# Performance work log

Measured on AMD Instinct MI355X. Metric: run time of the kernel, lower is better.

## Reference

```python
import jax, jax.numpy as jnp
import numpy as np

B, C, N = 8, 256, 2048

def setup_inputs() -> dict:
    key = jax.random.key(0)
    ks = jax.random.split(key, 7)
    s = 1.0 / np.sqrt(C)
    return {
        "x": jax.random.normal(ks[0], (B, C, N), dtype=jnp.float32),
        "Wq": jax.random.normal(ks[1], (C, C), dtype=jnp.float32) * s,
        "bq": jax.random.normal(ks[2], (C,), dtype=jnp.float32) * s,
        "Wk": jax.random.normal(ks[3], (C, C), dtype=jnp.float32) * s,
        "bk": jax.random.normal(ks[4], (C,), dtype=jnp.float32) * s,
        "Wv": jax.random.normal(ks[5], (C, C), dtype=jnp.float32) * s,
        "bv": jax.random.normal(ks[6], (C,), dtype=jnp.float32) * s,
    }

def reference(x, Wq, bq, Wk, bk, Wv, bv):
    # x: [B, C, N]; Conv1d(k=1) == channel-mixing matmul + bias
    q = jnp.einsum('oc,bcn->bon', Wq, x) + bq[None, :, None]  # [B,C,N]
    k = jnp.einsum('oc,bcn->bon', Wk, x) + bk[None, :, None]  # [B,C,N]
    v = jnp.einsum('oc,bcn->bon', Wv, x) + bv[None, :, None]  # [B,C,N]
    # qk = bmm(q^T, k): [B, N, N]
    qk = jnp.einsum('bcn,bcm->bnm', q, k)
    # global-sum normalization over the ENTIRE qk tensor (not row-wise softmax)
    attn_w = qk / jnp.sum(qk)
    # attn = bmm(v, attn_w): [B, C, N]
    attn = jnp.einsum('bcn,bnm->bcm', v, attn_w)
    return attn
```

## Files before the change

### kernel.cpp

```cpp
#include <hip/hip_runtime.h>


typedef _Float16 half8 __attribute__((ext_vector_type(8)));
typedef _Float16 half4 __attribute__((ext_vector_type(4)));
typedef _Float16 half2v __attribute__((ext_vector_type(2)));
typedef float f4v __attribute__((ext_vector_type(4)));

#define GP  40
#define GPB 36

__launch_bounds__(256)
__global__ void k1_kernel(const float* __restrict__ x, const float* __restrict__ Wq,
                          const float* __restrict__ Wk, const float* __restrict__ bq,
                          const float* __restrict__ bk, float* __restrict__ sxpart,
                          float* __restrict__ W3, float* __restrict__ u2,
                          float* __restrict__ w1, float* __restrict__ s1,
                          float* __restrict__ S, float* __restrict__ Gpart) {
    __shared__ __align__(16) char smem[40960];
    const int blk = blockIdx.x, t = threadIdx.x;
    if (blk < 192) {
        _Float16* Ah = (_Float16*)smem;
        _Float16* Al = Ah + 128 * GP;
        _Float16* Bh = Al + 128 * GP;
        _Float16* Bl = Bh + 128 * GP;
        const int tileId = blk >> 6;
        const int y = blk & 63;
        const int b = y >> 3, ks = y & 7;
        const int r0 = (tileId == 2) ? 128 : 0;
        const int c0 = (tileId == 0) ? 0 : 128;
        const bool diag = (tileId != 1);
        const float* xb = x + (long)b * 524288;

        const int lane = t & 63, wave = t >> 6;
        const int wy = wave >> 1, wx = wave & 1;
        const int mIn = lane & 15, quad = lane >> 4;

        f4v acc[4][4] = {};
        const int aBase = (wy * 64 + mIn) * GP + quad * 8;
        const int bBase = (wx * 64 + mIn) * GP + quad * 8;
        const int srow = t >> 3;
        const int skq  = (t & 7) * 4;
        float rs[4] = {};

        float4 pa[4], pb[4];
        int kk = ks * 256;
        #pragma unroll
        for (int i = 0; i < 4; ++i) {
            pa[i] = *(const float4*)&xb[(long)(r0 + srow + i * 32) * 2048 + kk + skq];
            if (!diag) pb[i] = *(const float4*)&xb[(long)(c0 + srow + i * 32) * 2048 + kk + skq];
        }

        for (int kb = 0; kb < 8; ++kb) {
            if (kb) __syncthreads();
            #pragma unroll
            for (int i = 0; i < 4; ++i) {
                const int row = srow + i * 32;
                half4 hv, lv;
                hv[0] = (_Float16)pa[i].x; lv[0] = (_Float16)(pa[i].x - (float)hv[0]);
                hv[1] = (_Float16)pa[i].y; lv[1] = (_Float16)(pa[i].y - (float)hv[1]);
                hv[2] = (_Float16)pa[i].z; lv[2] = (_Float16)(pa[i].z - (float)hv[2]);
                hv[3] = (_Float16)pa[i].w; lv[3] = (_Float16)(pa[i].w - (float)hv[3]);
                *(half4*)&Ah[row * GP + skq] = hv;
                *(half4*)&Al[row * GP + skq] = lv;
                if (diag) {
                    rs[i] += pa[i].x + pa[i].y + pa[i].z + pa[i].w;
                } else {
                    half4 hb, lb;
                    hb[0] = (_Float16)pb[i].x; lb[0] = (_Float16)(pb[i].x - (float)hb[0]);
                    hb[1] = (_Float16)pb[i].y; lb[1] = (_Float16)(pb[i].y - (float)hb[1]);
                    hb[2] = (_Float16)pb[i].z; lb[2] = (_Float16)(pb[i].z - (float)hb[2]);
                    hb[3] = (_Float16)pb[i].w; lb[3] = (_Float16)(pb[i].w - (float)hb[3]);
                    *(half4*)&Bh[row * GP + skq] = hb;
                    *(half4*)&Bl[row * GP + skq] = lb;
                }
            }
            __syncthreads();
            kk += 32;
            if (kb < 7) {
                #pragma unroll
                for (int i = 0; i < 4; ++i) {
                    pa[i] = *(const float4*)&xb[(long)(r0 + srow + i * 32) * 2048 + kk + skq];
                    if (!diag) pb[i] = *(const float4*)&xb[(long)(c0 + srow + i * 32) * 2048 + kk + skq];
                }
            }
            const _Float16* BhP = diag ? Ah : Bh;
            const _Float16* BlP = diag ? Al : Bl;
            #pragma unroll
            for (int ph = 0; ph < 3; ++ph) {
                const _Float16* As = (ph == 2) ? Al : Ah;
                const _Float16* Bs = (ph == 1) ? BlP : BhP;
                half8 af[4], bf[4];
                #pragma unroll
                for (int i = 0; i < 4; ++i) {
                    af[i] = *(const half8*)&As[aBase + i * 16 * GP];
                    bf[i] = *(const half8*)&Bs[bBase + i * 16 * GP];
                }
                #pragma unroll
                for (int i = 0; i < 4; ++i)
                    #pragma unroll
                    for (int j = 0; j < 4; ++j)
                        acc[i][j] = __builtin_amdgcn_mfma_f32_16x16x32_f16(af[i], bf[j], acc[i][j], 0, 0, 0);
            }
        }

        if (diag) {
            #pragma unroll
            for (int i = 0; i < 4; ++i) {
                rs[i] += __shfl_xor(rs[i], 1);
                rs[i] += __shfl_xor(rs[i], 2);
                rs[i] += __shfl_xor(rs[i], 4);
            }
            if ((t & 7) == 0) {
                #pragma unroll
                for (int i = 0; i < 4; ++i)
                    sxpart[ks * 2048 + b * 256 + r0 + srow + i * 32] = rs[i];
            }
        }

        float* D = Gpart + ((long)(ks * 8 + b) << 16);
        #pragma unroll
        for (int i = 0; i < 4; ++i)
            #pragma unroll
            for (int j = 0; j < 4; ++j) {
                const int row = r0 + wy * 64 + i * 16 + quad * 4;
                const int col = c0 + wx * 64 + j * 16 + mIn;
                #pragma unroll
                for (int r = 0; r < 4; ++r)
                    D[(row + r) * 256 + col] = acc[i][j][r];
                if (tileId == 1)
                    *(float4*)&D[(long)col * 256 + row] =
                        make_float4(acc[i][j][0], acc[i][j][1], acc[i][j][2], acc[i][j][3]);
            }
    } else if (blk < 208) {
        float* ldsA = (float*)smem;
        float* ldsB = ldsA + 16 * 68;
        const int tile = blk - 192;
        const int r0 = (tile >> 2) * 64, j0 = (tile & 3) * 64;
        const int tx = t & 15, ty = t >> 4;
        float acc[4][4] = {};
        for (int kk = 0; kk < 256; kk += 16) {
            *(float4*)&ldsA[ty * 68 + tx * 4] = *(const float4*)&Wq[(long)(kk + ty) * 256 + r0 + tx * 4];
            *(float4*)&ldsB[ty * 68 + tx * 4] = *(const float4*)&Wk[(long)(kk + ty) * 256 + j0 + tx * 4];
            __syncthreads();
            #pragma unroll
            for (int k = 0; k < 16; ++k) {
                const float4 av4 = *(const float4*)&ldsA[k * 68 + ty * 4];
                const float4 bv4 = *(const float4*)&ldsB[k * 68 + tx * 4];
                const float ar[4] = {av4.x, av4.y, av4.z, av4.w};
                const float br[4] = {bv4.x, bv4.y, bv4.z, bv4.w};
                #pragma unroll
                for (int i = 0; i < 4; ++i)
                    #pragma unroll
                    for (int j = 0; j < 4; ++j)
                        acc[i][j] = fmaf(ar[i], br[j], acc[i][j]);
            }
            __syncthreads();
        }
        #pragma unroll
        for (int i = 0; i < 4; ++i)
            *(float4*)&W3[(long)(r0 + ty * 4 + i) * 256 + j0 + tx * 4] =
                make_float4(acc[i][0], acc[i][1], acc[i][2], acc[i][3]);
    } else {
        float* sbq = (float*)smem;
        float* sbk = sbq + 256;
        float* red = sbk + 256;
        if (t == 0) S[0] = 0.0f;
        sbq[t] = bq[t]; sbk[t] = bk[t];
        __syncthreads();
        float u = 0.0f, w = 0.0f;
        #pragma unroll 8
        for (int c = 0; c < 256; ++c) {
            u = fmaf(Wk[(long)c * 256 + t], sbq[c], u);
            w = fmaf(Wq[(long)c * 256 + t], sbk[c], w);
        }
        u2[t] = u; w1[t] = w;
        red[t] = sbq[t] * sbk[t]; __syncthreads();
        for (int h = 128; h > 0; h >>= 1) { if (t < h) red[t] += red[t + h]; __syncthreads(); }
        if (t == 0) s1[0] = red[0];
    }
}

__launch_bounds__(256)
__global__ void k2_kernel(const float* __restrict__ Wv, const float* __restrict__ Gpart,
                          const float* __restrict__ W3, const float* __restrict__ u2,
                          const float* __restrict__ w1, const float* __restrict__ s1p,
                          const float* __restrict__ sxpart, float* __restrict__ T1,
                          float* __restrict__ v2, float* __restrict__ s2,
                          float* __restrict__ wvsx, float* __restrict__ S) {
    __shared__ __align__(16) char smem[40960];
    const int blk = blockIdx.x, t = threadIdx.x;
    if (blk < 256) {
        float* ldsA = (float*)smem;
        float* ldsB = ldsA + 32 * 34;
        const int r0 = (blk >> 5) * 32;
        const int g  = blk & 31;
        const int b  = g >> 2;
        const int j0 = (g & 3) * 64;
        const int tx = t & 15, ty = t >> 4;
        const int ar = t >> 3, ak4 = (t & 7) * 4;
        const float* Gb = Gpart + (long)b * 65536 + j0;
        float acc[2][4] = {};

        f4v pa, pg[2][8];
        pa = *(const f4v*)&Wv[(long)(r0 + ar) * 256 + ak4];
        #pragma unroll
        for (int s = 0; s < 2; ++s)
            #pragma unroll
            for (int ksl = 0; ksl < 8; ++ksl)
                pg[s][ksl] = *(const f4v*)&Gb[(long)ksl * 524288 + (long)(s * 16 + ty) * 256 + tx * 4];

        for (int c = 0; c < 8; ++c) {
            const int kk = c * 32;
            ldsA[(ak4 + 0) * 34 + ar] = pa[0];
            ldsA[(ak4 + 1) * 34 + ar] = pa[1];
            ldsA[(ak4 + 2) * 34 + ar] = pa[2];
            ldsA[(ak4 + 3) * 34 + ar] = pa[3];
            #pragma unroll
            for (int s = 0; s < 2; ++s) {
                f4v bs = pg[s][0];
                #pragma unroll
                for (int ksl = 1; ksl < 8; ++ksl) bs += pg[s][ksl];
                *(f4v*)&ldsB[(s * 16 + ty) * 68 + tx * 4] = bs;
            }
            __syncthreads();
            if (c < 7) {
                const int kn = kk + 32;
                pa = *(const f4v*)&Wv[(long)(r0 + ar) * 256 + kn + ak4];
                #pragma unroll
                for (int s = 0; s < 2; ++s)
                    #pragma unroll
                    for (int ksl = 0; ksl < 8; ++ksl)
                        pg[s][ksl] = *(const f4v*)&Gb[(long)ksl * 524288 + (long)(kn + s * 16 + ty) * 256 + tx * 4];
            }
            #pragma unroll
            for (int k = 0; k < 32; ++k) {
                const float2 av2 = *(const float2*)&ldsA[k * 34 + ty * 2];
                const float4 bv4 = *(const float4*)&ldsB[k * 68 + tx * 4];
                acc[0][0] = fmaf(av2.x, bv4.x, acc[0][0]);
                acc[0][1] = fmaf(av2.x, bv4.y, acc[0][1]);
                acc[0][2] = fmaf(av2.x, bv4.z, acc[0][2]);
                acc[0][3] = fmaf(av2.x, bv4.w, acc[0][3]);
                acc[1][0] = fmaf(av2.y, bv4.x, acc[1][0]);
                acc[1][1] = fmaf(av2.y, bv4.y, acc[1][1]);
                acc[1][2] = fmaf(av2.y, bv4.z, acc[1][2]);
                acc[1][3] = fmaf(av2.y, bv4.w, acc[1][3]);
            }
            __syncthreads();
        }
        float* D = T1 + (long)b * 65536;
        #pragma unroll
        for (int i = 0; i < 2; ++i)
            *(float4*)&D[(long)(r0 + ty * 2 + i) * 256 + j0 + tx * 4] =
                make_float4(acc[i][0], acc[i][1], acc[i][2], acc[i][3]);
    } else if (blk < 264) {
        float* ssx = (float*)smem;
        float* red = ssx + 256;
        const int b = blk - 256, j = t;
        float sxv = 0.0f;
        #pragma unroll
        for (int ks = 0; ks < 8; ++ks) sxv += sxpart[ks * 2048 + b * 256 + j];
        ssx[j] = sxv;
        __syncthreads();
        float vr = 0.0f;
        #pragma unroll 8
        for (int c = 0; c < 256; ++c) vr = fmaf(W3[(long)c * 256 + j], ssx[c], vr);
        const float v2j = vr + 2048.0f * u2[j];
        v2[b * 256 + j] = v2j;
        red[j] = v2j * sxv; __syncthreads();
        for (int h = 128; h > 0; h >>= 1) { if (j < h) red[j] += red[j + h]; __syncthreads(); }
        const float sd1 = red[0];
        __syncthreads();
        red[j] = sxv * w1[j]; __syncthreads();
        for (int h = 128; h > 0; h >>= 1) { if (j < h) red[j] += red[j + h]; __syncthreads(); }
        if (j == 0) {
            const float s2v = red[0] + 2048.0f * s1p[0];
            s2[b] = s2v;
            atomicAdd(S, sd1 + 2048.0f * s2v);
        }
    } else {
        float* wtile = (float*)smem;
        float* sxs = wtile + 8192;
        const int r0w = (blk - 264) * 32;
        #pragma unroll
        for (int p = 0; p < 8; ++p) {
            const int f = t + p * 256;
            const int row = f >> 6, c4 = f & 63;
            *(float4*)&wtile[row * 256 + c4 * 4] = *(const float4*)&Wv[(long)(r0w + row) * 256 + c4 * 4];
        }
        #pragma unroll
        for (int p = 0; p < 8; ++p) {
            const int f = t + p * 256;
            float s = 0.0f;
            #pragma unroll
            for (int ks = 0; ks < 8; ++ks) s += sxpart[ks * 2048 + f];
            sxs[f] = s;
        }
        __syncthreads();
        const int r = t >> 3, q = t & 7;
        float acc[8] = {};
        for (int ci = 0; ci < 32; ++ci) {
            const float wv = wtile[r * 256 + q * 32 + ci];
            #pragma unroll
            for (int b = 0; b < 8; ++b) acc[b] = fmaf(wv, sxs[b * 256 + q * 32 + ci], acc[b]);
        }
        #pragma unroll
        for (int b = 0; b < 8; ++b) {
            acc[b] += __shfl_xor(acc[b], 1);
            acc[b] += __shfl_xor(acc[b], 2);
            acc[b] += __shfl_xor(acc[b], 4);
        }
        if (q == 0) {
            #pragma unroll
            for (int b = 0; b < 8; ++b) wvsx[b * 256 + r0w + r] = acc[b];
        }
    }
}

__launch_bounds__(256)
__global__ void ap_kernel(const float* __restrict__ T1, const float* __restrict__ W3,
                          const float* __restrict__ wvsx, const float* __restrict__ u2,
                          const float* __restrict__ bv, const float* __restrict__ v2,
                          const float* __restrict__ w1, const float* __restrict__ s1p,
                          const float* __restrict__ s2, _Float16* __restrict__ Aph,
                          _Float16* __restrict__ Apl, float* __restrict__ cvec) {
    __shared__ __align__(16) float ldsA[32 * 34];
    __shared__ __align__(16) float ldsB[32 * 68];
    __shared__ float sw1[256];
    const int b = blockIdx.z;
    const int r0 = blockIdx.y * 32, j0 = blockIdx.x * 64;
    const float* A = T1 + (long)b * 65536;
    const int t = threadIdx.x, tx = t & 15, ty = t >> 4;
    const int ar = t >> 3, ak4 = (t & 7) * 4;
    sw1[t] = w1[t];
    float acc[2][4] = {};
    float dot[2] = {};

    f4v pa, pb[2];
    pa = *(const f4v*)&A[(long)(r0 + ar) * 256 + ak4];
    pb[0] = *(const f4v*)&W3[(long)(ty) * 256 + j0 + tx * 4];
    pb[1] = *(const f4v*)&W3[(long)(16 + ty) * 256 + j0 + tx * 4];

    for (int c = 0; c < 8; ++c) {
        const int kk = c * 32;
        ldsA[(ak4 + 0) * 34 + ar] = pa[0];
        ldsA[(ak4 + 1) * 34 + ar] = pa[1];
        ldsA[(ak4 + 2) * 34 + ar] = pa[2];
        ldsA[(ak4 + 3) * 34 + ar] = pa[3];
        *(f4v*)&ldsB[ty * 68 + tx * 4] = pb[0];
        *(f4v*)&ldsB[(16 + ty) * 68 + tx * 4] = pb[1];
        __syncthreads();
        if (c < 7) {
            const int kn = kk + 32;
            pa = *(const f4v*)&A[(long)(r0 + ar) * 256 + kn + ak4];
            pb[0] = *(const f4v*)&W3[(long)(kn + ty) * 256 + j0 + tx * 4];
            pb[1] = *(const f4v*)&W3[(long)(kn + 16 + ty) * 256 + j0 + tx * 4];
        }
        #pragma unroll
        for (int k = 0; k < 32; ++k) {
            const float2 av2 = *(const float2*)&ldsA[k * 34 + ty * 2];
            const float4 bv4 = *(const float4*)&ldsB[k * 68 + tx * 4];
            const float wk = sw1[kk + k];
            dot[0] = fmaf(av2.x, wk, dot[0]);
            dot[1] = fmaf(av2.y, wk, dot[1]);
            acc[0][0] = fmaf(av2.x, bv4.x, acc[0][0]);
            acc[0][1] = fmaf(av2.x, bv4.y, acc[0][1]);
            acc[0][2] = fmaf(av2.x, bv4.z, acc[0][2]);
            acc[0][3] = fmaf(av2.x, bv4.w, acc[0][3]);
            acc[1][0] = fmaf(av2.y, bv4.x, acc[1][0]);
            acc[1][1] = fmaf(av2.y, bv4.y, acc[1][1]);
            acc[1][2] = fmaf(av2.y, bv4.z, acc[1][2]);
            acc[1][3] = fmaf(av2.y, bv4.w, acc[1][3]);
        }
        __syncthreads();
    }
    #pragma unroll
    for (int i = 0; i < 2; ++i) {
        const int r = r0 + ty * 2 + i;
        const float e1 = wvsx[b * 256 + r], e3 = bv[r];
        half4 hv, lv;
        #pragma unroll
        for (int j = 0; j < 4; ++j) {
            const int col = j0 + tx * 4 + j;
            const float val = acc[i][j] + e1 * u2[col] + e3 * v2[b * 256 + col];
            hv[j] = (_Float16)val;
            lv[j] = (_Float16)(val - (float)hv[j]);
        }
        const long o = (long)b * 65536 + (long)r * 256 + j0 + tx * 4;
        *(half4*)&Aph[o] = hv;
        *(half4*)&Apl[o] = lv;
        if (j0 == 0 && tx == 0)
            cvec[b * 256 + r] = dot[i] + e1 * s1p[0] + e3 * s2[b];
    }
}

__launch_bounds__(256)
__global__ void gemmF_mfma(const _Float16* __restrict__ Aph, const _Float16* __restrict__ Apl,
                           const float* __restrict__ x, const float* __restrict__ Sptr,
                           const float* __restrict__ cvec, float* __restrict__ out) {
    __shared__ __align__(16) _Float16 Ah[128 * GP];
    __shared__ __align__(16) _Float16 Al[128 * GP];
    __shared__ __align__(16) _Float16 Bh[128 * GPB];
    __shared__ __align__(16) _Float16 Bl[128 * GPB];
    __shared__ __align__(16) float xt[32 * 132];

    const int n0 = blockIdx.x * 128;
    const int c0 = blockIdx.y * 128;
    const int b = blockIdx.z;
    const _Float16* Asrc_h = Aph + (long)b * 65536;
    const _Float16* Asrc_l = Apl + (long)b * 65536;
    const float* xb = x + (long)b * 524288;

    const int t = threadIdx.x;
    const int lane = t & 63, wave = t >> 6;
    const int wy = wave >> 1, wx = wave & 1;
    const int mIn = lane & 15, quad = lane >> 4;

    f4v acc[4][4] = {};
    const int aBase = (wy * 64 + mIn) * GP + quad * 8;
    const int bBase = (wx * 64 + mIn) * GPB + quad * 8;
    const int cn = t & 127;
    const int ckh = (t >> 7) * 16;

    int arow[2], ako[2], xk[4], xn[4];
    #pragma unroll
    for (int i = 0; i < 2; ++i) { const int idx = t + (i << 8); arow[i] = idx >> 2; ako[i] = (idx & 3) << 3; }
    #pragma unroll
    for (int p = 0; p < 4; ++p) { const int f = t + p * 256; xk[p] = f >> 5; xn[p] = f & 31; }

    uint4 pah[2], pal[2]; f4v px[4];
    #pragma unroll
    for (int i = 0; i < 2; ++i) {
        pah[i] = *(const uint4*)&Asrc_h[(long)(c0 + arow[i]) * 256 + ako[i]];
        pal[i] = *(const uint4*)&Asrc_l[(long)(c0 + arow[i]) * 256 + ako[i]];
    }
    #pragma unroll
    for (int p = 0; p < 4; ++p)
        px[p] = *(const f4v*)&xb[(long)xk[p] * 2048 + n0 + xn[p] * 4];

    for (int kk = 0; kk < 256; kk += 32) {
        #pragma unroll
        for (int i = 0; i < 2; ++i) {
            *(uint4*)&Ah[arow[i] * GP + ako[i]] = pah[i];
            *(uint4*)&Al[arow[i] * GP + ako[i]] = pal[i];
        }
        #pragma unroll
        for (int p = 0; p < 4; ++p)
            *(f4v*)&xt[xk[p] * 132 + xn[p] * 4] = px[p];
        __syncthreads();
        {
            _Float16 hs[16], ls[16];
            #pragma unroll
            for (int k = 0; k < 16; ++k) {
                const float v = xt[(ckh + k) * 132 + cn];
                hs[k] = (_Float16)v;
                ls[k] = (_Float16)(v - (float)hs[k]);
            }
            #pragma unroll
            for (int k2 = 0; k2 < 8; ++k2) {
                half2v h2; h2[0] = hs[2 * k2]; h2[1] = hs[2 * k2 + 1];
                half2v l2; l2[0] = ls[2 * k2]; l2[1] = ls[2 * k2 + 1];
                *(half2v*)&Bh[cn * GPB + ckh + 2 * k2] = h2;
                *(half2v*)&Bl[cn * GPB + ckh + 2 * k2] = l2;
            }
        }
        __syncthreads();
        if (kk < 224) {
            const int kn = kk + 32;
            #pragma unroll
            for (int i = 0; i < 2; ++i) {
                pah[i] = *(const uint4*)&Asrc_h[(long)(c0 + arow[i]) * 256 + kn + ako[i]];
                pal[i] = *(const uint4*)&Asrc_l[(long)(c0 + arow[i]) * 256 + kn + ako[i]];
            }
            #pragma unroll
            for (int p = 0; p < 4; ++p)
                px[p] = *(const f4v*)&xb[(long)(kn + xk[p]) * 2048 + n0 + xn[p] * 4];
        }
        #pragma unroll
        for (int ph = 0; ph < 3; ++ph) {
            const _Float16* As = (ph == 2) ? Al : Ah;
            const _Float16* Bs = (ph == 1) ? Bl : Bh;
            half8 af[4], bf[4];
            #pragma unroll
            for (int i = 0; i < 4; ++i) {
                af[i] = *(const half8*)&As[aBase + i * 16 * GP];
                const half4 b0 = *(const half4*)&Bs[bBase + i * 16 * GPB];
                const half4 b1 = *(const half4*)&Bs[bBase + i * 16 * GPB + 4];
                bf[i] = __builtin_shufflevector(b0, b1, 0, 1, 2, 3, 4, 5, 6, 7);
            }
            #pragma unroll
            for (int i = 0; i < 4; ++i)
                #pragma unroll
                for (int j = 0; j < 4; ++j)
                    acc[i][j] = __builtin_amdgcn_mfma_f32_16x16x32_f16(af[i], bf[j], acc[i][j], 0, 0, 0);
        }
        __syncthreads();
    }

    const float invS = 1.0f / Sptr[0];
    float* ob = out + (long)b * 524288;
    const float* cv = cvec + b * 256;
    #pragma unroll
    for (int i = 0; i < 4; ++i)
        #pragma unroll
        for (int r = 0; r < 4; ++r) {
            const int row = c0 + wy * 64 + i * 16 + quad * 4 + r;
            const float c = cv[row];
            #pragma unroll
            for (int j = 0; j < 4; ++j) {
                const int col = n0 + wx * 64 + j * 16 + mIn;
                ob[(long)row * 2048 + col] = (acc[i][j][r] + c) * invS;
            }
        }
}

extern "C" void kernel_launch(void* const* d_in, const int* in_sizes, int n_in,
                              void* d_out, int out_size, void* d_ws, size_t ws_size,
                              hipStream_t stream) {
    const float* x  = (const float*)d_in[0];
    const float* Wq = (const float*)d_in[1];
    const float* bq = (const float*)d_in[2];
    const float* Wk = (const float*)d_in[3];
    const float* bk = (const float*)d_in[4];
    const float* Wv = (const float*)d_in[5];
    const float* bv = (const float*)d_in[6];
    float* out = (float*)d_out;
    float* ws  = (float*)d_ws;

    float* T1     = ws;
    float* W3     = ws + 524288;
    float* sxpart = ws + 589824;
    float* wvsx   = ws + 606208;
    float* v2     = ws + 608256;
    float* cvec   = ws + 610304;
    float* s2     = ws + 612352;
    float* u2     = ws + 612360;
    float* w1     = ws + 612616;
    float* s1     = ws + 612872;
    float* S      = ws + 612873;
    float* Gpart  = ws + 612880;
    _Float16* Aph = (_Float16*)(ws + 4807184);
    _Float16* Apl = Aph + 524288;

    k1_kernel<<<dim3(209), 256, 0, stream>>>(x, Wq, Wk, bq, bk, sxpart, W3, u2, w1, s1, S, Gpart);
    k2_kernel<<<dim3(272), 256, 0, stream>>>(Wv, Gpart, W3, u2, w1, s1, sxpart, T1, v2, s2, wvsx, S);
    ap_kernel<<<dim3(4, 8, 8), 256, 0, stream>>>(T1, W3, wvsx, u2, bv, v2, w1, s1, s2, Aph, Apl, cvec);
    gemmF_mfma<<<dim3(16, 2, 8), 256, 0, stream>>>(Aph, Apl, x, S, cvec, out);
}
```

Baseline: 154.3 us.

## Fuse four kernels into one persistent kernel with software grid barriers

Merges the four stage kernels into a single 256-block kernel whose phases are separated by atomic-counter grid barriers, with a memset resetting the barrier flags each launch. The aim is to remove the launch gaps and tail drain between the short dependent stages. The cost is that every block must be co-resident (256 blocks on 256 CUs), blocks spin while waiting, and stages with fewer blocks, such as the reduction ones, leave most of the grid idle at each barrier.

```diff
diff --git a/kernel.cpp b/kernel.cpp
--- a/kernel.cpp
+++ b/kernel.cpp
@@ -9,15 +9,38 @@
 #define GP  40
 #define GPB 36
 
-__launch_bounds__(256)
-__global__ void k1_kernel(const float* __restrict__ x, const float* __restrict__ Wq,
-                          const float* __restrict__ Wk, const float* __restrict__ bq,
-                          const float* __restrict__ bk, float* __restrict__ sxpart,
-                          float* __restrict__ W3, float* __restrict__ u2,
-                          float* __restrict__ w1, float* __restrict__ s1,
-                          float* __restrict__ S, float* __restrict__ Gpart) {
-    __shared__ __align__(16) char smem[40960];
+__device__ __forceinline__ void gbar(unsigned* cnt, unsigned* flag, unsigned nblk) {
+    __syncthreads();
+    if (threadIdx.x == 0) {
+        __threadfence();
+        if (__hip_atomic_fetch_add(cnt, 1u, __ATOMIC_RELAXED, __HIP_MEMORY_SCOPE_AGENT) == nblk - 1u) {
+            __hip_atomic_store(flag, 1u, __ATOMIC_RELAXED, __HIP_MEMORY_SCOPE_AGENT);
+        } else {
+            while (__hip_atomic_load(flag, __ATOMIC_RELAXED, __HIP_MEMORY_SCOPE_AGENT) == 0u)
+                __builtin_amdgcn_s_sleep(2);
+        }
+        __threadfence();
+    }
+    __syncthreads();
+}
+
+__launch_bounds__(256, 1)
+__global__ void fused_kernel(const float* __restrict__ x, const float* __restrict__ Wq,
+                             const float* __restrict__ bq, const float* __restrict__ Wk,
+                             const float* __restrict__ bk, const float* __restrict__ Wv,
+                             const float* __restrict__ bv, float* __restrict__ out,
+                             float* __restrict__ T1, float* __restrict__ W3,
+                             float* __restrict__ sxpart, float* __restrict__ wvsx,
+                             float* __restrict__ v2, float* __restrict__ cvec,
+                             float* __restrict__ s2, float* __restrict__ u2,
+                             float* __restrict__ w1, float* __restrict__ s1,
+                             float* __restrict__ S, float* __restrict__ Gpart,
+                             _Float16* __restrict__ Aph, _Float16* __restrict__ Apl,
+                             unsigned* __restrict__ bar) {
+    __shared__ __align__(16) char smem[55808];
     const int blk = blockIdx.x, t = threadIdx.x;
+    const unsigned NBLK = 256;
+
     if (blk < 192) {
         _Float16* Ah = (_Float16*)smem;
         _Float16* Al = Ah + 128 * GP;
@@ -160,7 +183,7 @@
         for (int i = 0; i < 4; ++i)
             *(float4*)&W3[(long)(r0 + ty * 4 + i) * 256 + j0 + tx * 4] =
                 make_float4(acc[i][0], acc[i][1], acc[i][2], acc[i][3]);
-    } else {
+    } else if (blk == 208) {
         float* sbq = (float*)smem;
         float* sbk = sbq + 256;
         float* red = sbk + 256;
@@ -178,18 +201,10 @@
         for (int h = 128; h > 0; h >>= 1) { if (t < h) red[t] += red[t + h]; __syncthreads(); }
         if (t == 0) s1[0] = red[0];
     }
-}
-
-__launch_bounds__(256)
-__global__ void k2_kernel(const float* __restrict__ Wv, const float* __restrict__ Gpart,
-                          const float* __restrict__ W3, const float* __restrict__ u2,
-                          const float* __restrict__ w1, const float* __restrict__ s1p,
-                          const float* __restrict__ sxpart, float* __restrict__ T1,
-                          float* __restrict__ v2, float* __restrict__ s2,
-                          float* __restrict__ wvsx, float* __restrict__ S) {
-    __shared__ __align__(16) char smem[40960];
-    const int blk = blockIdx.x, t = threadIdx.x;
-    if (blk < 256) {
+
+    gbar(&bar[0], &bar[1], NBLK);
+
+    {
         float* ldsA = (float*)smem;
         float* ldsB = ldsA + 32 * 34;
         const int r0 = (blk >> 5) * 32;
@@ -252,10 +267,12 @@
         for (int i = 0; i < 2; ++i)
             *(float4*)&D[(long)(r0 + ty * 2 + i) * 256 + j0 + tx * 4] =
                 make_float4(acc[i][0], acc[i][1], acc[i][2], acc[i][3]);
-    } else if (blk < 264) {
+    }
+    if (blk < 8) {
+        __syncthreads();
         float* ssx = (float*)smem;
         float* red = ssx + 256;
-        const int b = blk - 256, j = t;
+        const int b = blk, j = t;
         float sxv = 0.0f;
         #pragma unroll
         for (int ks = 0; ks < 8; ++ks) sxv += sxpart[ks * 2048 + b * 256 + j];
@@ -273,14 +290,15 @@
         red[j] = sxv * w1[j]; __syncthreads();
         for (int h = 128; h > 0; h >>= 1) { if (j < h) red[j] += red[j + h]; __syncthreads(); }
         if (j == 0) {
-            const float s2v = red[0] + 2048.0f * s1p[0];
+            const float s2v = red[0] + 2048.0f * s1[0];
             s2[b] = s2v;
             atomicAdd(S, sd1 + 2048.0f * s2v);
         }
-    } else {
+    } else if (blk < 16) {
+        __syncthreads();
         float* wtile = (float*)smem;
         float* sxs = wtile + 8192;
-        const int r0w = (blk - 264) * 32;
+        const int r0w = (blk - 8) * 32;
         #pragma unroll
         for (int p = 0; p < 8; ++p) {
             const int f = t + p * 256;
@@ -314,203 +332,197 @@
             for (int b = 0; b < 8; ++b) wvsx[b * 256 + r0w + r] = acc[b];
         }
     }
-}
-
-__launch_bounds__(256)
-__global__ void ap_kernel(const float* __restrict__ T1, const float* __restrict__ W3,
-                          const float* __restrict__ wvsx, const float* __restrict__ u2,
-                          const float* __restrict__ bv, const float* __restrict__ v2,
-                          const float* __restrict__ w1, const float* __restrict__ s1p,
-                          const float* __restrict__ s2, _Float16* __restrict__ Aph,
-                          _Float16* __restrict__ Apl, float* __restrict__ cvec) {
-    __shared__ __align__(16) float ldsA[32 * 34];
-    __shared__ __align__(16) float ldsB[32 * 68];
-    __shared__ float sw1[256];
-    const int b = blockIdx.z;
-    const int r0 = blockIdx.y * 32, j0 = blockIdx.x * 64;
-    const float* A = T1 + (long)b * 65536;
-    const int t = threadIdx.x, tx = t & 15, ty = t >> 4;
-    const int ar = t >> 3, ak4 = (t & 7) * 4;
-    sw1[t] = w1[t];
-    float acc[2][4] = {};
-    float dot[2] = {};
-
-    f4v pa, pb[2];
-    pa = *(const f4v*)&A[(long)(r0 + ar) * 256 + ak4];
-    pb[0] = *(const f4v*)&W3[(long)(ty) * 256 + j0 + tx * 4];
-    pb[1] = *(const f4v*)&W3[(long)(16 + ty) * 256 + j0 + tx * 4];
-
-    for (int c = 0; c < 8; ++c) {
-        const int kk = c * 32;
-        ldsA[(ak4 + 0) * 34 + ar] = pa[0];
-        ldsA[(ak4 + 1) * 34 + ar] = pa[1];
-        ldsA[(ak4 + 2) * 34 + ar] = pa[2];
-        ldsA[(ak4 + 3) * 34 + ar] = pa[3];
-        *(f4v*)&ldsB[ty * 68 + tx * 4] = pb[0];
-        *(f4v*)&ldsB[(16 + ty) * 68 + tx * 4] = pb[1];
-        __syncthreads();
-        if (c < 7) {
-            const int kn = kk + 32;
-            pa = *(const f4v*)&A[(long)(r0 + ar) * 256 + kn + ak4];
-            pb[0] = *(const f4v*)&W3[(long)(kn + ty) * 256 + j0 + tx * 4];
-            pb[1] = *(const f4v*)&W3[(long)(kn + 16 + ty) * 256 + j0 + tx * 4];
-        }
-        #pragma unroll
-        for (int k = 0; k < 32; ++k) {
-            const float2 av2 = *(const float2*)&ldsA[k * 34 + ty * 2];
-            const float4 bv4 = *(const float4*)&ldsB[k * 68 + tx * 4];
-            const float wk = sw1[kk + k];
-            dot[0] = fmaf(av2.x, wk, dot[0]);
-            dot[1] = fmaf(av2.y, wk, dot[1]);
-            acc[0][0] = fmaf(av2.x, bv4.x, acc[0][0]);
-            acc[0][1] = fmaf(av2.x, bv4.y, acc[0][1]);
-            acc[0][2] = fmaf(av2.x, bv4.z, acc[0][2]);
-            acc[0][3] = fmaf(av2.x, bv4.w, acc[0][3]);
-            acc[1][0] = fmaf(av2.y, bv4.x, acc[1][0]);
-            acc[1][1] = fmaf(av2.y, bv4.y, acc[1][1]);
-            acc[1][2] = fmaf(av2.y, bv4.z, acc[1][2]);
-            acc[1][3] = fmaf(av2.y, bv4.w, acc[1][3]);
-        }
-        __syncthreads();
+
+    gbar(&bar[2], &bar[3], NBLK);
+
+    {
+        float* ldsA = (float*)smem;
+        float* ldsB = (float*)(smem + 4352);
+        float* sw1  = (float*)(smem + 13056);
+        const int b  = blk >> 5;
+        const int r0 = ((blk >> 2) & 7) * 32, j0 = (blk & 3) * 64;
+        const float* A = T1 + (long)b * 65536;
+        const int tx = t & 15, ty = t >> 4;
+        const int ar = t >> 3, ak4 = (t & 7) * 4;
+        sw1[t] = w1[t];
+        float acc[2][4] = {};
+        float dot[2] = {};
+
+        f4v pa, pb[2];
+        pa = *(const f4v*)&A[(long)(r0 + ar) * 256 + ak4];
+        pb[0] = *(const f4v*)&W3[(long)(ty) * 256 + j0 + tx * 4];
+        pb[1] = *(const f4v*)&W3[(long)(16 + ty) * 256 + j0 + tx * 4];
+
+        for (int c = 0; c < 8; ++c) {
+            const int kk = c * 32;
+            ldsA[(ak4 + 0) * 34 + ar] = pa[0];
+            ldsA[(ak4 + 1) * 34 + ar] = pa[1];
+            ldsA[(ak4 + 2) * 34 + ar] = pa[2];
+            ldsA[(ak4 + 3) * 34 + ar] = pa[3];
+            *(f4v*)&ldsB[ty * 68 + tx * 4] = pb[0];
+            *(f4v*)&ldsB[(16 + ty) * 68 + tx * 4] = pb[1];
+            __syncthreads();
+            if (c < 7) {
+                const int kn = kk + 32;
+                pa = *(const f4v*)&A[(long)(r0 + ar) * 256 + kn + ak4];
+                pb[0] = *(const f4v*)&W3[(long)(kn + ty) * 256 + j0 + tx * 4];
+                pb[1] = *(const f4v*)&W3[(long)(kn + 16 + ty) * 256 + j0 + tx * 4];
+            }
+            #pragma unroll
+            for (int k = 0; k < 32; ++k) {
+                const float2 av2 = *(const float2*)&ldsA[k * 34 + ty * 2];
+                const float4 bv4 = *(const float4*)&ldsB[k * 68 + tx * 4];
+                const float wk = sw1[kk + k];
+                dot[0] = fmaf(av2.x, wk, dot[0]);
+                dot[1] = fmaf(av2.y, wk, dot[1]);
+                acc[0][0] = fmaf(av2.x, bv4.x, acc[0][0]);
+                acc[0][1] = fmaf(av2.x, bv4.y, acc[0][1]);
+                acc[0][2] = fmaf(av2.x, bv4.z, acc[0][2]);
+                acc[0][3] = fmaf(av2.x, bv4.w, acc[0][3]);
+                acc[1][0] = fmaf(av2.y, bv4.x, acc[1][0]);
+                acc[1][1] = fmaf(av2.y, bv4.y, acc[1][1]);
+                acc[1][2] = fmaf(av2.y, bv4.z, acc[1][2]);
+                acc[1][3] = fmaf(av2.y, bv4.w, acc[1][3]);
+            }
+            __syncthreads();
+        }
+        #pragma unroll
+        for (int i = 0; i < 2; ++i) {
+            const int r = r0 + ty * 2 + i;
+            const float e1 = wvsx[b * 256 + r], e3 = bv[r];
+            half4 hv, lv;
+            #pragma unroll
+            for (int j = 0; j < 4; ++j) {
+                const int col = j0 + tx * 4 + j;
+                const float val = acc[i][j] + e1 * u2[col] + e3 * v2[b * 256 + col];
+                hv[j] = (_Float16)val;
+                lv[j] = (_Float16)(val - (float)hv[j]);
+            }
+            const long o = (long)b * 65536 + (long)r * 256 + j0 + tx * 4;
+            *(half4*)&Aph[o] = hv;
+            *(half4*)&Apl[o] = lv;
+            if (j0 == 0 && tx == 0)
+                cvec[b * 256 + r] = dot[i] + e1 * s1[0] + e3 * s2[b];
+        }
     }
-    #pragma unroll
-    for (int i = 0; i < 2; ++i) {
-        const int r = r0 + ty * 2 + i;
-        const float e1 = wvsx[b * 256 + r], e3 = bv[r];
-        half4 hv, lv;
-        #pragma unroll
-        for (int j = 0; j < 4; ++j) {
-            const int col = j0 + tx * 4 + j;
-            const float val = acc[i][j] + e1 * u2[col] + e3 * v2[b * 256 + col];
-            hv[j] = (_Float16)val;
-            lv[j] = (_Float16)(val - (float)hv[j]);
-        }
-        const long o = (long)b * 65536 + (long)r * 256 + j0 + tx * 4;
-        *(half4*)&Aph[o] = hv;
-        *(half4*)&Apl[o] = lv;
-        if (j0 == 0 && tx == 0)
-            cvec[b * 256 + r] = dot[i] + e1 * s1p[0] + e3 * s2[b];
+
+    gbar(&bar[4], &bar[5], NBLK);
+
+    {
+        _Float16* Ah = (_Float16*)smem;
+        _Float16* Al = (_Float16*)(smem + 10240);
+        _Float16* Bh = (_Float16*)(smem + 20480);
+        _Float16* Bl = (_Float16*)(smem + 29696);
+        float*    xt = (float*)(smem + 38912);
+
+        const int n0 = (blk & 15) * 128;
+        const int c0 = ((blk >> 4) & 1) * 128;
+        const int b  = blk >> 5;
+        const _Float16* Asrc_h = Aph + (long)b * 65536;
+        const _Float16* Asrc_l = Apl + (long)b * 65536;
+        const float* xb = x + (long)b * 524288;
+
+        const int lane = t & 63, wave = t >> 6;
+        const int wy = wave >> 1, wx = wave & 1;
+        const int mIn = lane & 15, quad = lane >> 4;
+
+        f4v acc[4][4] = {};
+        const int aBase = (wy * 64 + mIn) * GP + quad * 8;
+        const int bBase = (wx * 64 + mIn) * GPB + quad * 8;
+        const int cn = t & 127;
+        const int ckh = (t >> 7) * 16;
+
+        int arow[2], ako[2], xk[4], xn[4];
+        #pragma unroll
+        for (int i = 0; i < 2; ++i) { const int idx = t + (i << 8); arow[i] = idx >> 2; ako[i] = (idx & 3) << 3; }
+        #pragma unroll
+        for (int p = 0; p < 4; ++p) { const int f = t + p * 256; xk[p] = f >> 5; xn[p] = f & 31; }
+
+        uint4 pah[2], pal[2]; f4v px[4];
+        #pragma unroll
+        for (int i = 0; i < 2; ++i) {
+            pah[i] = *(const uint4*)&Asrc_h[(long)(c0 + arow[i]) * 256 + ako[i]];
+            pal[i] = *(const uint4*)&Asrc_l[(long)(c0 + arow[i]) * 256 + ako[i]];
+        }
+        #pragma unroll
+        for (int p = 0; p < 4; ++p)
+            px[p] = *(const f4v*)&xb[(long)xk[p] * 2048 + n0 + xn[p] * 4];
+
+        for (int kk = 0; kk < 256; kk += 32) {
+            #pragma unroll
+            for (int i = 0; i < 2; ++i) {
+                *(uint4*)&Ah[arow[i] * GP + ako[i]] = pah[i];
+                *(uint4*)&Al[arow[i] * GP + ako[i]] = pal[i];
+            }
+            #pragma unroll
+            for (int p = 0; p < 4; ++p)
+                *(f4v*)&xt[xk[p] * 132 + xn[p] * 4] = px[p];
+            __syncthreads();
+            {
+                _Float16 hs[16], ls[16];
+                #pragma unroll
+                for (int k = 0; k < 16; ++k) {
+                    const float v = xt[(ckh + k) * 132 + cn];
+                    hs[k] = (_Float16)v;
+                    ls[k] = (_Float16)(v - (float)hs[k]);
+                }
+                #pragma unroll
+                for (int k2 = 0; k2 < 8; ++k2) {
+                    half2v h2; h2[0] = hs[2 * k2]; h2[1] = hs[2 * k2 + 1];
+                    half2v l2; l2[0] = ls[2 * k2]; l2[1] = ls[2 * k2 + 1];
+                    *(half2v*)&Bh[cn * GPB + ckh + 2 * k2] = h2;
+                    *(half2v*)&Bl[cn * GPB + ckh + 2 * k2] = l2;
+                }
+            }
+            __syncthreads();
+            if (kk < 224) {
+                const int kn = kk + 32;
+                #pragma unroll
+                for (int i = 0; i < 2; ++i) {
+                    pah[i] = *(const uint4*)&Asrc_h[(long)(c0 + arow[i]) * 256 + kn + ako[i]];
+                    pal[i] = *(const uint4*)&Asrc_l[(long)(c0 + arow[i]) * 256 + kn + ako[i]];
+                }
+                #pragma unroll
+                for (int p = 0; p < 4; ++p)
+                    px[p] = *(const f4v*)&xb[(long)(kn + xk[p]) * 2048 + n0 + xn[p] * 4];
+            }
+            #pragma unroll
+            for (int ph = 0; ph < 3; ++ph) {
+                const _Float16* As = (ph == 2) ? Al : Ah;
+                const _Float16* Bs = (ph == 1) ? Bl : Bh;
+                half8 af[4], bf[4];
+                #pragma unroll
+                for (int i = 0; i < 4; ++i) {
+                    af[i] = *(const half8*)&As[aBase + i * 16 * GP];
+                    const half4 b0 = *(const half4*)&Bs[bBase + i * 16 * GPB];
+                    const half4 b1 = *(const half4*)&Bs[bBase + i * 16 * GPB + 4];
+                    bf[i] = __builtin_shufflevector(b0, b1, 0, 1, 2, 3, 4, 5, 6, 7);
+                }
+                #pragma unroll
+                for (int i = 0; i < 4; ++i)
+                    #pragma unroll
+                    for (int j = 0; j < 4; ++j)
+                        acc[i][j] = __builtin_amdgcn_mfma_f32_16x16x32_f16(af[i], bf[j], acc[i][j], 0, 0, 0);
+            }
+            __syncthreads();
+        }
+
+        const float invS = 1.0f / S[0];
+        float* ob = out + (long)b * 524288;
+        const float* cv = cvec + b * 256;
+        #pragma unroll
+        for (int i = 0; i < 4; ++i)
+            #pragma unroll
+            for (int r = 0; r < 4; ++r) {
+                const int row = c0 + wy * 64 + i * 16 + quad * 4 + r;
+                const float c = cv[row];
+                #pragma unroll
+                for (int j = 0; j < 4; ++j) {
+                    const int col = n0 + wx * 64 + j * 16 + mIn;
+                    ob[(long)row * 2048 + col] = (acc[i][j][r] + c) * invS;
+                }
+            }
     }
-}
-
-__launch_bounds__(256)
-__global__ void gemmF_mfma(const _Float16* __restrict__ Aph, const _Float16* __restrict__ Apl,
-                           const float* __restrict__ x, const float* __restrict__ Sptr,
-                           const float* __restrict__ cvec, float* __restrict__ out) {
-    __shared__ __align__(16) _Float16 Ah[128 * GP];
-    __shared__ __align__(16) _Float16 Al[128 * GP];
-    __shared__ __align__(16) _Float16 Bh[128 * GPB];
-    __shared__ __align__(16) _Float16 Bl[128 * GPB];
-    __shared__ __align__(16) float xt[32 * 132];
-
-    const int n0 = blockIdx.x * 128;
-    const int c0 = blockIdx.y * 128;
-    const int b = blockIdx.z;
-    const _Float16* Asrc_h = Aph + (long)b * 65536;
-    const _Float16* Asrc_l = Apl + (long)b * 65536;
-    const float* xb = x + (long)b * 524288;
-
-    const int t = threadIdx.x;
-    const int lane = t & 63, wave = t >> 6;
-    const int wy = wave >> 1, wx = wave & 1;
-    const int mIn = lane & 15, quad = lane >> 4;
-
-    f4v acc[4][4] = {};
-    const int aBase = (wy * 64 + mIn) * GP + quad * 8;
-    const int bBase = (wx * 64 + mIn) * GPB + quad * 8;
-    const int cn = t & 127;
-    const int ckh = (t >> 7) * 16;
-
-    int arow[2], ako[2], xk[4], xn[4];
-    #pragma unroll
-    for (int i = 0; i < 2; ++i) { const int idx = t + (i << 8); arow[i] = idx >> 2; ako[i] = (idx & 3) << 3; }
-    #pragma unroll
-    for (int p = 0; p < 4; ++p) { const int f = t + p * 256; xk[p] = f >> 5; xn[p] = f & 31; }
-
-    uint4 pah[2], pal[2]; f4v px[4];
-    #pragma unroll
-    for (int i = 0; i < 2; ++i) {
-        pah[i] = *(const uint4*)&Asrc_h[(long)(c0 + arow[i]) * 256 + ako[i]];
-        pal[i] = *(const uint4*)&Asrc_l[(long)(c0 + arow[i]) * 256 + ako[i]];
-    }
-    #pragma unroll
-    for (int p = 0; p < 4; ++p)
-        px[p] = *(const f4v*)&xb[(long)xk[p] * 2048 + n0 + xn[p] * 4];
-
-    for (int kk = 0; kk < 256; kk += 32) {
-        #pragma unroll
-        for (int i = 0; i < 2; ++i) {
-            *(uint4*)&Ah[arow[i] * GP + ako[i]] = pah[i];
-            *(uint4*)&Al[arow[i] * GP + ako[i]] = pal[i];
-        }
-        #pragma unroll
-        for (int p = 0; p < 4; ++p)
-            *(f4v*)&xt[xk[p] * 132 + xn[p] * 4] = px[p];
-        __syncthreads();
-        {
-            _Float16 hs[16], ls[16];
-            #pragma unroll
-            for (int k = 0; k < 16; ++k) {
-                const float v = xt[(ckh + k) * 132 + cn];
-                hs[k] = (_Float16)v;
-                ls[k] = (_Float16)(v - (float)hs[k]);
-            }
-            #pragma unroll
-            for (int k2 = 0; k2 < 8; ++k2) {
-                half2v h2; h2[0] = hs[2 * k2]; h2[1] = hs[2 * k2 + 1];
-                half2v l2; l2[0] = ls[2 * k2]; l2[1] = ls[2 * k2 + 1];
-                *(half2v*)&Bh[cn * GPB + ckh + 2 * k2] = h2;
-                *(half2v*)&Bl[cn * GPB + ckh + 2 * k2] = l2;
-            }
-        }
-        __syncthreads();
-        if (kk < 224) {
-            const int kn = kk + 32;
-            #pragma unroll
-            for (int i = 0; i < 2; ++i) {
-                pah[i] = *(const uint4*)&Asrc_h[(long)(c0 + arow[i]) * 256 + kn + ako[i]];
-                pal[i] = *(const uint4*)&Asrc_l[(long)(c0 + arow[i]) * 256 + kn + ako[i]];
-            }
-            #pragma unroll
-            for (int p = 0; p < 4; ++p)
-                px[p] = *(const f4v*)&xb[(long)(kn + xk[p]) * 2048 + n0 + xn[p] * 4];
-        }
-        #pragma unroll
-        for (int ph = 0; ph < 3; ++ph) {
-            const _Float16* As = (ph == 2) ? Al : Ah;
-            const _Float16* Bs = (ph == 1) ? Bl : Bh;
-            half8 af[4], bf[4];
-            #pragma unroll
-            for (int i = 0; i < 4; ++i) {
-                af[i] = *(const half8*)&As[aBase + i * 16 * GP];
-                const half4 b0 = *(const half4*)&Bs[bBase + i * 16 * GPB];
-                const half4 b1 = *(const half4*)&Bs[bBase + i * 16 * GPB + 4];
-                bf[i] = __builtin_shufflevector(b0, b1, 0, 1, 2, 3, 4, 5, 6, 7);
-            }
-            #pragma unroll
-            for (int i = 0; i < 4; ++i)
-                #pragma unroll
-                for (int j = 0; j < 4; ++j)
-                    acc[i][j] = __builtin_amdgcn_mfma_f32_16x16x32_f16(af[i], bf[j], acc[i][j], 0, 0, 0);
-        }
-        __syncthreads();
-    }
-
-    const float invS = 1.0f / Sptr[0];
-    float* ob = out + (long)b * 524288;
-    const float* cv = cvec + b * 256;
-    #pragma unroll
-    for (int i = 0; i < 4; ++i)
-        #pragma unroll
-        for (int r = 0; r < 4; ++r) {
-            const int row = c0 + wy * 64 + i * 16 + quad * 4 + r;
-            const float c = cv[row];
-            #pragma unroll
-            for (int j = 0; j < 4; ++j) {
-                const int col = n0 + wx * 64 + j * 16 + mIn;
-                ob[(long)row * 2048 + col] = (acc[i][j][r] + c) * invS;
-            }
-        }
 }
 
 extern "C" void kernel_launch(void* const* d_in, const int* in_sizes, int n_in,
@@ -540,9 +552,11 @@
     float* Gpart  = ws + 612880;
     _Float16* Aph = (_Float16*)(ws + 4807184);
     _Float16* Apl = Aph + 524288;
-
-    k1_kernel<<<dim3(209), 256, 0, stream>>>(x, Wq, Wk, bq, bk, sxpart, W3, u2, w1, s1, S, Gpart);
-    k2_kernel<<<dim3(272), 256, 0, stream>>>(Wv, Gpart, W3, u2, w1, s1, sxpart, T1, v2, s2, wvsx, S);
-    ap_kernel<<<dim3(4, 8, 8), 256, 0, stream>>>(T1, W3, wvsx, u2, bv, v2, w1, s1, s2, Aph, Apl, cvec);
-    gemmF_mfma<<<dim3(16, 2, 8), 256, 0, stream>>>(Aph, Apl, x, S, cvec, out);
+    unsigned* bar = (unsigned*)(ws + 5331472);
+
+    hipMemsetAsync(bar, 0, 64, stream);
+
+    fused_kernel<<<dim3(256), dim3(256), 0, stream>>>(
+        x, Wq, bq, Wk, bk, Wv, bv, out,
+        T1, W3, sxpart, wvsx, v2, cvec, s2, u2, w1, s1, S, Gpart, Aph, Apl, bar);
 }
```

New measurement: 210.4 us. 36.4% more time.

## Halve GEMM tile widths to double block counts and reorder small blocks first

Applied to the files above, without the earlier changes.

The Gram-matrix blocks in k1 now compute 128x64 output tiles instead of 128x128, doubling the GEMM block count from 192 to 384. The small side-task blocks move to the front of the grid in k1 and k2. The final gemmF kernel likewise halves its N tile to 64, launching 512 blocks instead of 256. The aim is better occupancy and fuller CU coverage on a 256-CU part, at the cost of more redundant A-tile loading and fp16 splitting per block, and lower MFMA reuse per block.

```diff
diff --git a/kernel.cpp b/kernel.cpp
--- a/kernel.cpp
+++ b/kernel.cpp
@@ -16,38 +16,45 @@
                           float* __restrict__ W3, float* __restrict__ u2,
                           float* __restrict__ w1, float* __restrict__ s1,
                           float* __restrict__ S, float* __restrict__ Gpart) {
-    __shared__ __align__(16) char smem[40960];
+    __shared__ __align__(16) char smem[30720];
     const int blk = blockIdx.x, t = threadIdx.x;
-    if (blk < 192) {
+    if (blk >= 17) {
         _Float16* Ah = (_Float16*)smem;
         _Float16* Al = Ah + 128 * GP;
         _Float16* Bh = Al + 128 * GP;
-        _Float16* Bl = Bh + 128 * GP;
-        const int tileId = blk >> 6;
-        const int y = blk & 63;
+        _Float16* Bl = Bh + 64 * GP;
+        const int gb = blk - 17;
+        const int sub = gb >> 6;
+        const int y = gb & 63;
         const int b = y >> 3, ks = y & 7;
+        const int tileId = sub >> 1, ch = sub & 1;
         const int r0 = (tileId == 2) ? 128 : 0;
-        const int c0 = (tileId == 0) ? 0 : 128;
+        const int c0 = ((tileId == 0) ? 0 : 128) + ch * 64;
         const bool diag = (tileId != 1);
+        const bool doRS = diag && (ch == 0);
         const float* xb = x + (long)b * 524288;
 
         const int lane = t & 63, wave = t >> 6;
         const int wy = wave >> 1, wx = wave & 1;
         const int mIn = lane & 15, quad = lane >> 4;
 
-        f4v acc[4][4] = {};
+        f4v acc[4][2] = {};
         const int aBase = (wy * 64 + mIn) * GP + quad * 8;
-        const int bBase = (wx * 64 + mIn) * GP + quad * 8;
+        const int bBase = diag ? ((ch * 64 + wx * 32 + mIn) * GP + quad * 8)
+                               : ((wx * 32 + mIn) * GP + quad * 8);
         const int srow = t >> 3;
         const int skq  = (t & 7) * 4;
         float rs[4] = {};
 
-        float4 pa[4], pb[4];
+        float4 pa[4], pb[2];
         int kk = ks * 256;
         #pragma unroll
-        for (int i = 0; i < 4; ++i) {
+        for (int i = 0; i < 4; ++i)
             pa[i] = *(const float4*)&xb[(long)(r0 + srow + i * 32) * 2048 + kk + skq];
-            if (!diag) pb[i] = *(const float4*)&xb[(long)(c0 + srow + i * 32) * 2048 + kk + skq];
+        if (!diag) {
+            #pragma unroll
+            for (int i = 0; i < 2; ++i)
+                pb[i] = *(const float4*)&xb[(long)(c0 + srow + i * 32) * 2048 + kk + skq];
         }
 
         for (int kb = 0; kb < 8; ++kb) {
@@ -62,9 +69,12 @@
                 hv[3] = (_Float16)pa[i].w; lv[3] = (_Float16)(pa[i].w - (float)hv[3]);
                 *(half4*)&Ah[row * GP + skq] = hv;
                 *(half4*)&Al[row * GP + skq] = lv;
-                if (diag) {
-                    rs[i] += pa[i].x + pa[i].y + pa[i].z + pa[i].w;
-                } else {
+                if (doRS) rs[i] += pa[i].x + pa[i].y + pa[i].z + pa[i].w;
+            }
+            if (!diag) {
+                #pragma unroll
+                for (int i = 0; i < 2; ++i) {
+                    const int row = srow + i * 32;
                     half4 hb, lb;
                     hb[0] = (_Float16)pb[i].x; lb[0] = (_Float16)(pb[i].x - (float)hb[0]);
                     hb[1] = (_Float16)pb[i].y; lb[1] = (_Float16)(pb[i].y - (float)hb[1]);
@@ -78,9 +88,12 @@
             kk += 32;
             if (kb < 7) {
                 #pragma unroll
-                for (int i = 0; i < 4; ++i) {
+                for (int i = 0; i < 4; ++i)
                     pa[i] = *(const float4*)&xb[(long)(r0 + srow + i * 32) * 2048 + kk + skq];
-                    if (!diag) pb[i] = *(const float4*)&xb[(long)(c0 + srow + i * 32) * 2048 + kk + skq];
+                if (!diag) {
+                    #pragma unroll
+                    for (int i = 0; i < 2; ++i)
+                        pb[i] = *(const float4*)&xb[(long)(c0 + srow + i * 32) * 2048 + kk + skq];
                 }
             }
             const _Float16* BhP = diag ? Ah : Bh;
@@ -89,21 +102,22 @@
             for (int ph = 0; ph < 3; ++ph) {
                 const _Float16* As = (ph == 2) ? Al : Ah;
                 const _Float16* Bs = (ph == 1) ? BlP : BhP;
-                half8 af[4], bf[4];
-                #pragma unroll
-                for (int i = 0; i < 4; ++i) {
+                half8 af[4], bf[2];
+                #pragma unroll
+                for (int i = 0; i < 4; ++i)
                     af[i] = *(const half8*)&As[aBase + i * 16 * GP];
-                    bf[i] = *(const half8*)&Bs[bBase + i * 16 * GP];
-                }
+                #pragma unroll
+                for (int j = 0; j < 2; ++j)
+                    bf[j] = *(const half8*)&Bs[bBase + j * 16 * GP];
                 #pragma unroll
                 for (int i = 0; i < 4; ++i)
                     #pragma unroll
-                    for (int j = 0; j < 4; ++j)
+                    for (int j = 0; j < 2; ++j)
                         acc[i][j] = __builtin_amdgcn_mfma_f32_16x16x32_f16(af[i], bf[j], acc[i][j], 0, 0, 0);
             }
         }
 
-        if (diag) {
+        if (doRS) {
             #pragma unroll
             for (int i = 0; i < 4; ++i) {
                 rs[i] += __shfl_xor(rs[i], 1);
@@ -121,9 +135,9 @@
         #pragma unroll
         for (int i = 0; i < 4; ++i)
             #pragma unroll
-            for (int j = 0; j < 4; ++j) {
+            for (int j = 0; j < 2; ++j) {
                 const int row = r0 + wy * 64 + i * 16 + quad * 4;
-                const int col = c0 + wx * 64 + j * 16 + mIn;
+                const int col = c0 + wx * 32 + j * 16 + mIn;
                 #pragma unroll
                 for (int r = 0; r < 4; ++r)
                     D[(row + r) * 256 + col] = acc[i][j][r];
@@ -131,10 +145,10 @@
                     *(float4*)&D[(long)col * 256 + row] =
                         make_float4(acc[i][j][0], acc[i][j][1], acc[i][j][2], acc[i][j][3]);
             }
-    } else if (blk < 208) {
+    } else if (blk < 16) {
         float* ldsA = (float*)smem;
         float* ldsB = ldsA + 16 * 68;
-        const int tile = blk - 192;
+        const int tile = blk;
         const int r0 = (tile >> 2) * 64, j0 = (tile & 3) * 64;
         const int tx = t & 15, ty = t >> 4;
         float acc[4][4] = {};
@@ -189,11 +203,12 @@
                           float* __restrict__ wvsx, float* __restrict__ S) {
     __shared__ __align__(16) char smem[40960];
     const int blk = blockIdx.x, t = threadIdx.x;
-    if (blk < 256) {
+    if (blk >= 16) {
         float* ldsA = (float*)smem;
         float* ldsB = ldsA + 32 * 34;
-        const int r0 = (blk >> 5) * 32;
-        const int g  = blk & 31;
+        const int gb = blk - 16;
+        const int r0 = (gb >> 5) * 32;
+        const int g  = gb & 31;
         const int b  = g >> 2;
         const int j0 = (g & 3) * 64;
         const int tx = t & 15, ty = t >> 4;
@@ -252,10 +267,10 @@
         for (int i = 0; i < 2; ++i)
             *(float4*)&D[(long)(r0 + ty * 2 + i) * 256 + j0 + tx * 4] =
                 make_float4(acc[i][0], acc[i][1], acc[i][2], acc[i][3]);
-    } else if (blk < 264) {
+    } else if (blk < 8) {
         float* ssx = (float*)smem;
         float* red = ssx + 256;
-        const int b = blk - 256, j = t;
+        const int b = blk, j = t;
         float sxv = 0.0f;
         #pragma unroll
         for (int ks = 0; ks < 8; ++ks) sxv += sxpart[ks * 2048 + b * 256 + j];
@@ -280,7 +295,7 @@
     } else {
         float* wtile = (float*)smem;
         float* sxs = wtile + 8192;
-        const int r0w = (blk - 264) * 32;
+        const int r0w = (blk - 8) * 32;
         #pragma unroll
         for (int p = 0; p < 8; ++p) {
             const int f = t + p * 256;
@@ -399,11 +414,11 @@
                            const float* __restrict__ cvec, float* __restrict__ out) {
     __shared__ __align__(16) _Float16 Ah[128 * GP];
     __shared__ __align__(16) _Float16 Al[128 * GP];
-    __shared__ __align__(16) _Float16 Bh[128 * GPB];
-    __shared__ __align__(16) _Float16 Bl[128 * GPB];
-    __shared__ __align__(16) float xt[32 * 132];
-
-    const int n0 = blockIdx.x * 128;
+    __shared__ __align__(16) _Float16 Bh[64 * GPB];
+    __shared__ __align__(16) _Float16 Bl[64 * GPB];
+    __shared__ __align__(16) float xt[32 * 68];
+
+    const int n0 = blockIdx.x * 64;
     const int c0 = blockIdx.y * 128;
     const int b = blockIdx.z;
     const _Float16* Asrc_h = Aph + (long)b * 65536;
@@ -415,26 +430,26 @@
     const int wy = wave >> 1, wx = wave & 1;
     const int mIn = lane & 15, quad = lane >> 4;
 
-    f4v acc[4][4] = {};
+    f4v acc[4][2] = {};
     const int aBase = (wy * 64 + mIn) * GP + quad * 8;
-    const int bBase = (wx * 64 + mIn) * GPB + quad * 8;
-    const int cn = t & 127;
-    const int ckh = (t >> 7) * 16;
-
-    int arow[2], ako[2], xk[4], xn[4];
+    const int bBase = (wx * 32 + mIn) * GPB + quad * 8;
+    const int cn = t & 63;
+    const int ck = (t >> 6) * 8;
+
+    int arow[2], ako[2], xk[2], xn[2];
     #pragma unroll
     for (int i = 0; i < 2; ++i) { const int idx = t + (i << 8); arow[i] = idx >> 2; ako[i] = (idx & 3) << 3; }
     #pragma unroll
-    for (int p = 0; p < 4; ++p) { const int f = t + p * 256; xk[p] = f >> 5; xn[p] = f & 31; }
-
-    uint4 pah[2], pal[2]; f4v px[4];
+    for (int p = 0; p < 2; ++p) { const int f = t + p * 256; xk[p] = f >> 4; xn[p] = f & 15; }
+
+    uint4 pah[2], pal[2]; f4v px[2];
     #pragma unroll
     for (int i = 0; i < 2; ++i) {
         pah[i] = *(const uint4*)&Asrc_h[(long)(c0 + arow[i]) * 256 + ako[i]];
         pal[i] = *(const uint4*)&Asrc_l[(long)(c0 + arow[i]) * 256 + ako[i]];
     }
     #pragma unroll
-    for (int p = 0; p < 4; ++p)
+    for (int p = 0; p < 2; ++p)
         px[p] = *(const f4v*)&xb[(long)xk[p] * 2048 + n0 + xn[p] * 4];
 
     for (int kk = 0; kk < 256; kk += 32) {
@@ -444,23 +459,23 @@
             *(uint4*)&Al[arow[i] * GP + ako[i]] = pal[i];
         }
         #pragma unroll
-        for (int p = 0; p < 4; ++p)
-            *(f4v*)&xt[xk[p] * 132 + xn[p] * 4] = px[p];
+        for (int p = 0; p < 2; ++p)
+            *(f4v*)&xt[xk[p] * 68 + xn[p] * 4] = px[p];
         __syncthreads();
         {
-            _Float16 hs[16], ls[16];
-            #pragma unroll
-            for (int k = 0; k < 16; ++k) {
-                const float v = xt[(ckh + k) * 132 + cn];
+            _Float16 hs[8], ls[8];
+            #pragma unroll
+            for (int k = 0; k < 8; ++k) {
+                const float v = xt[(ck + k) * 68 + cn];
                 hs[k] = (_Float16)v;
                 ls[k] = (_Float16)(v - (float)hs[k]);
             }
             #pragma unroll
-            for (int k2 = 0; k2 < 8; ++k2) {
+            for (int k2 = 0; k2 < 4; ++k2) {
                 half2v h2; h2[0] = hs[2 * k2]; h2[1] = hs[2 * k2 + 1];
                 half2v l2; l2[0] = ls[2 * k2]; l2[1] = ls[2 * k2 + 1];
-                *(half2v*)&Bh[cn * GPB + ckh + 2 * k2] = h2;
-                *(half2v*)&Bl[cn * GPB + ckh + 2 * k2] = l2;
+                *(half2v*)&Bh[cn * GPB + ck + 2 * k2] = h2;
+                *(half2v*)&Bl[cn * GPB + ck + 2 * k2] = l2;
             }
         }
         __syncthreads();
@@ -472,25 +487,27 @@
                 pal[i] = *(const uint4*)&Asrc_l[(long)(c0 + arow[i]) * 256 + kn + ako[i]];
             }
             #pragma unroll
-            for (int p = 0; p < 4; ++p)
+            for (int p = 0; p < 2; ++p)
                 px[p] = *(const f4v*)&xb[(long)(kn + xk[p]) * 2048 + n0 + xn[p] * 4];
         }
         #pragma unroll
         for (int ph = 0; ph < 3; ++ph) {
             const _Float16* As = (ph == 2) ? Al : Ah;
             const _Float16* Bs = (ph == 1) ? Bl : Bh;
-            half8 af[4], bf[4];
-            #pragma unroll
-            for (int i = 0; i < 4; ++i) {
+            half8 af[4], bf[2];
+            #pragma unroll
+            for (int i = 0; i < 4; ++i)
                 af[i] = *(const half8*)&As[aBase + i * 16 * GP];
-                const half4 b0 = *(const half4*)&Bs[bBase + i * 16 * GPB];
-                const half4 b1 = *(const half4*)&Bs[bBase + i * 16 * GPB + 4];
-                bf[i] = __builtin_shufflevector(b0, b1, 0, 1, 2, 3, 4, 5, 6, 7);
+            #pragma unroll
+            for (int j = 0; j < 2; ++j) {
+                const half4 b0 = *(const half4*)&Bs[bBase + j * 16 * GPB];
+                const half4 b1 = *(const half4*)&Bs[bBase + j * 16 * GPB + 4];
+                bf[j] = __builtin_shufflevector(b0, b1, 0, 1, 2, 3, 4, 5, 6, 7);
             }
             #pragma unroll
             for (int i = 0; i < 4; ++i)
                 #pragma unroll
-                for (int j = 0; j < 4; ++j)
+                for (int j = 0; j < 2; ++j)
                     acc[i][j] = __builtin_amdgcn_mfma_f32_16x16x32_f16(af[i], bf[j], acc[i][j], 0, 0, 0);
         }
         __syncthreads();
@@ -506,8 +523,8 @@
             const int row = c0 + wy * 64 + i * 16 + quad * 4 + r;
             const float c = cv[row];
             #pragma unroll
-            for (int j = 0; j < 4; ++j) {
-                const int col = n0 + wx * 64 + j * 16 + mIn;
+            for (int j = 0; j < 2; ++j) {
+                const int col = n0 + wx * 32 + j * 16 + mIn;
                 ob[(long)row * 2048 + col] = (acc[i][j][r] + c) * invS;
             }
         }
@@ -541,8 +558,8 @@
     _Float16* Aph = (_Float16*)(ws + 4807184);
     _Float16* Apl = Aph + 524288;
 
-    k1_kernel<<<dim3(209), 256, 0, stream>>>(x, Wq, Wk, bq, bk, sxpart, W3, u2, w1, s1, S, Gpart);
+    k1_kernel<<<dim3(401), 256, 0, stream>>>(x, Wq, Wk, bq, bk, sxpart, W3, u2, w1, s1, S, Gpart);
     k2_kernel<<<dim3(272), 256, 0, stream>>>(Wv, Gpart, W3, u2, w1, s1, sxpart, T1, v2, s2, wvsx, S);
     ap_kernel<<<dim3(4, 8, 8), 256, 0, stream>>>(T1, W3, wvsx, u2, bv, v2, w1, s1, s2, Aph, Apl, cvec);
-    gemmF_mfma<<<dim3(16, 2, 8), 256, 0, stream>>>(Aph, Apl, x, S, cvec, out);
+    gemmF_mfma<<<dim3(32, 2, 8), 256, 0, stream>>>(Aph, Apl, x, S, cvec, out);
 }
```

Result: faster. 144.9 us (-6.1%).
